# Performance work log

Measured on AMD Instinct MI355X. Metric: run time of the kernel, lower is better.

Reference implementation:

```python
import jax, jax.numpy as jnp
import numpy as np

B, N = 16, 131072
C_MID, C_OUT = 128, 16


def setup_inputs() -> dict:
    key = jax.random.key(0)
    k1, k2, k3, k4 = jax.random.split(key, 4)
    # points in roughly [-0.5, 0.5] so cube indexing covers the grids
    x = jax.random.uniform(k1, (B, N, 3), dtype=jnp.float32) - 0.5
    W1 = jax.random.normal(k2, (C_MID, 3), dtype=jnp.float32) * 0.1
    b1 = jnp.zeros((C_MID,), jnp.float32)
    W2 = jax.random.normal(k3, (C_OUT, C_MID), dtype=jnp.float32) * 0.1
    b2 = jnp.zeros((C_OUT,), jnp.float32)
    # fixed per-batch permutations (deterministic stand-in for torch.randperm)
    perm = jnp.stack([jax.random.permutation(jax.random.fold_in(k4, i), N)
                      for i in range(B)]).astype(jnp.int32)
    return {"x": x, "W1": W1, "b1": b1, "W2": W2, "b2": b2, "perm": perm}


def point_to_cell(pts, feat, W, H, D):
    # pts float [B,N,3] already clamped to [0, dim-1]; cast like torch LongTensor
    idx = pts.astype(jnp.int32)
    flat = (idx[..., 0] * H + idx[..., 1]) * D + idx[..., 2]  # [B,N]
    Bb, Nn, C = feat.shape

    def scatter_one(fi, fe):
        grid = jnp.zeros((W * H * D, C), feat.dtype)
        return grid.at[fi].set(fe)

    cell = jax.vmap(scatter_one)(flat, feat)           # [B, WHD, C]
    return cell.transpose(0, 2, 1).reshape(Bb, C, W, H, D)


def reference(x, W1, b1, W2, b2, perm):
    # PointNetfeatLocal: 1x1 Conv1d stack == per-point MLP 3 -> 128 -> 16
    h = jnp.maximum(jnp.einsum('bnc,hc->bnh', x, W1) + b1, 0.0)
    feat = jnp.einsum('bnh,oh->bno', h, W2) + b2       # [B,N,16]
    # shuffle_points_feat: per-batch permutation gather
    xs = jnp.take_along_axis(x, perm[..., None], axis=1)
    fs = jnp.take_along_axis(feat, perm[..., None], axis=1)
    # batch_grid_pooling32 / 64
    cube32 = jnp.clip(xs * 32.0 + 16.5, 0.0, 31.0)
    cube64 = jnp.clip(xs * 64.0 + 32.5, 0.0, 63.0)
    feat_cell32 = point_to_cell(cube32, fs, 32, 32, 32)  # [B,16,32,32,32]
    feat_cell64 = point_to_cell(cube64, fs, 64, 64, 64)  # [B,16,64,64,64]
    return feat_cell32, feat_cell64
```

## Files before the change

### kernel.cpp

```cpp
#include <hip/hip_runtime.h>

namespace {
constexpr int kB = 16;
constexpr int kN = 131072;
constexpr int kNLog = 17;
constexpr int kCMid = 128;
constexpr int kCOut = 16;
constexpr int kCells32Log = 15;
constexpr int kCells64Log = 18;
constexpr int kCells32 = 1 << kCells32Log;
constexpr int kCells64 = 1 << kCells64Log;
constexpr long kOut32Elems = (long)kB * kCOut * kCells32;
constexpr int kChunks32 = 16;
constexpr int kSlabs64 = 16;
constexpr int kSlabCells = kCells64 / kSlabs64;
}

typedef __bf16 bf16x8 __attribute__((ext_vector_type(8)));
typedef float f32x4 __attribute__((ext_vector_type(4)));

__device__ inline unsigned int packbf2(float lo, float hi) {
    unsigned int a = __float_as_uint(lo);
    unsigned int b = __float_as_uint(hi);
    a = (a + 0x7FFFu + ((a >> 16) & 1u)) >> 16;
    b = (b + 0x7FFFu + ((b >> 16) & 1u)) & 0xFFFF0000u;
    return b | a;
}
__device__ inline float bf_lo(unsigned int p) { return __uint_as_float(p << 16); }
__device__ inline float bf_hi(unsigned int p) { return __uint_as_float(p & 0xFFFF0000u); }

__device__ inline uint4 pack8(const float* h) {
    uint4 r;
    r.x = packbf2(h[0], h[1]); r.y = packbf2(h[2], h[3]);
    r.z = packbf2(h[4], h[5]); r.w = packbf2(h[6], h[7]);
    return r;
}

__global__ __launch_bounds__(256) void k_pack(
    const float* __restrict__ W1, const float* __restrict__ b1,
    const float* __restrict__ W2,
    float* __restrict__ W1p, uint4* __restrict__ w2h, uint4* __restrict__ w2l)
{
    const int t = threadIdx.x;
    for (int k = t; k < kCMid; k += 256) {
        W1p[k * 4 + 0] = W1[k * 3 + 0];
        W1p[k * 4 + 1] = W1[k * 3 + 1];
        W1p[k * 4 + 2] = W1[k * 3 + 2];
        W1p[k * 4 + 3] = b1[k];
    }
    {
        const int kw = t >> 6;
        const int lane = t & 63;
        const int ch = lane & 15;
        const int grp = lane >> 4;
        float v[8], lo[8];
        #pragma unroll
        for (int e = 0; e < 8; ++e)
            v[e] = W2[ch * kCMid + kw * 32 + grp * 8 + e];
        const uint4 hh = pack8(v);
        lo[0] = v[0] - bf_lo(hh.x); lo[1] = v[1] - bf_hi(hh.x);
        lo[2] = v[2] - bf_lo(hh.y); lo[3] = v[3] - bf_hi(hh.y);
        lo[4] = v[4] - bf_lo(hh.z); lo[5] = v[5] - bf_hi(hh.z);
        lo[6] = v[6] - bf_lo(hh.w); lo[7] = v[7] - bf_hi(hh.w);
        w2h[t] = hh;
        w2l[t] = pack8(lo);
    }
}

__global__ __launch_bounds__(256) void k_prec(
    const float* __restrict__ x,
    const int* __restrict__ perm,
    unsigned long long* __restrict__ prec)
{
    const long gid = (long)blockIdx.x * 256 + threadIdx.x;
    const long bbase = gid & ~(long)(kN - 1);
    const int i = (int)(gid & (kN - 1));
    const int j = perm[gid];

    const float* xp = x + (bbase + j) * 3;
    const float v0 = xp[0], v1 = xp[1], v2 = xp[2];

    const int ix32 = (int)fminf(fmaxf(__fadd_rn(__fmul_rn(v0, 32.0f), 16.5f), 0.0f), 31.0f);
    const int iy32 = (int)fminf(fmaxf(__fadd_rn(__fmul_rn(v1, 32.0f), 16.5f), 0.0f), 31.0f);
    const int iz32 = (int)fminf(fmaxf(__fadd_rn(__fmul_rn(v2, 32.0f), 16.5f), 0.0f), 31.0f);
    const int ix64 = (int)fminf(fmaxf(__fadd_rn(__fmul_rn(v0, 64.0f), 32.5f), 0.0f), 63.0f);
    const int iy64 = (int)fminf(fmaxf(__fadd_rn(__fmul_rn(v1, 64.0f), 32.5f), 0.0f), 63.0f);
    const int iz64 = (int)fminf(fmaxf(__fadd_rn(__fmul_rn(v2, 64.0f), 32.5f), 0.0f), 63.0f);

    const unsigned long long cell32 = (unsigned long long)((ix32 * 32 + iy32) * 32 + iz32);
    const unsigned long long cell64 = (unsigned long long)((ix64 * 64 + iy64) * 64 + iz64);
    prec[bbase + j] = (cell64 << 33) | (cell32 << 18) | (unsigned long long)(i + 1);
}

__global__ __launch_bounds__(256, 4) void k_mlp(
    const float* __restrict__ x,
    const float* __restrict__ W1p,
    const uint4* __restrict__ w2h, const uint4* __restrict__ w2l,
    const float* __restrict__ b2,
    uint2* __restrict__ feat)
{
    const int tid = threadIdx.x;
    const int lane = tid & 63;
    const int grp = lane >> 4;
    const int pt16 = lane & 15;
    const long base = (((long)blockIdx.x << 2) + (tid >> 6)) << 6;

    float xv[4][3];
    #pragma unroll
    for (int t = 0; t < 4; ++t) {
        const float* xp = x + (base + t * 16 + pt16) * 3;
        xv[t][0] = xp[0]; xv[t][1] = xp[1]; xv[t][2] = xp[2];
    }

    f32x4 acc[4];
    #pragma unroll
    for (int t = 0; t < 4; ++t) acc[t] = (f32x4){0.f, 0.f, 0.f, 0.f};

    const float4* __restrict__ w1v = (const float4*)W1p;

    #pragma unroll
    for (int kw = 0; kw < 4; ++kw) {
        const bf16x8 ah = __builtin_bit_cast(bf16x8, w2h[(kw << 6) + lane]);
        const bf16x8 al = __builtin_bit_cast(bf16x8, w2l[(kw << 6) + lane]);
        float4 w1r[8];
        #pragma unroll
        for (int e = 0; e < 8; ++e)
            w1r[e] = w1v[(kw << 5) + (grp << 3) + e];

        #pragma unroll
        for (int t = 0; t < 4; ++t) {
            float h[8], lo[8];
            #pragma unroll
            for (int e = 0; e < 8; ++e)
                h[e] = fmaxf(fmaf(w1r[e].x, xv[t][0],
                              fmaf(w1r[e].y, xv[t][1],
                               fmaf(w1r[e].z, xv[t][2], w1r[e].w))), 0.0f);
            const uint4 bh = pack8(h);
            lo[0] = h[0] - bf_lo(bh.x); lo[1] = h[1] - bf_hi(bh.x);
            lo[2] = h[2] - bf_lo(bh.y); lo[3] = h[3] - bf_hi(bh.y);
            lo[4] = h[4] - bf_lo(bh.z); lo[5] = h[5] - bf_hi(bh.z);
            lo[6] = h[6] - bf_lo(bh.w); lo[7] = h[7] - bf_hi(bh.w);
            const uint4 bl4 = pack8(lo);
            const bf16x8 bhv = __builtin_bit_cast(bf16x8, bh);
            const bf16x8 blv = __builtin_bit_cast(bf16x8, bl4);
            acc[t] = __builtin_amdgcn_mfma_f32_16x16x32_bf16(ah, bhv, acc[t], 0, 0, 0);
            acc[t] = __builtin_amdgcn_mfma_f32_16x16x32_bf16(ah, blv, acc[t], 0, 0, 0);
            acc[t] = __builtin_amdgcn_mfma_f32_16x16x32_bf16(al, bhv, acc[t], 0, 0, 0);
        }
    }

    const float4 bias = ((const float4*)b2)[grp];
    #pragma unroll
    for (int t = 0; t < 4; ++t) {
        const float c0 = acc[t][0] + bias.x;
        const float c1 = acc[t][1] + bias.y;
        const float c2 = acc[t][2] + bias.z;
        const float c3 = acc[t][3] + bias.w;
        uint2 o;
        o.x = packbf2(c0, c1);
        o.y = packbf2(c2, c3);
        feat[((base + t * 16 + pt16) << 2) + grp] = o;
    }
}

__global__ __launch_bounds__(1024) void k_win32(
    const unsigned long long* __restrict__ prec,
    unsigned int* __restrict__ partial32)
{
    __shared__ unsigned int lwin[kCells32];
    const int b = blockIdx.x >> 4;
    const int c = blockIdx.x & (kChunks32 - 1);
    const int t = threadIdx.x;

    #pragma unroll
    for (int r = 0; r < kCells32 / 1024; ++r) lwin[r * 1024 + t] = 0u;
    __syncthreads();

    const long base = ((long)b << kNLog) + (long)c * (kN / kChunks32);
    #pragma unroll
    for (int r = 0; r < (kN / kChunks32) / 1024; ++r) {
        const unsigned long long w = prec[base + r * 1024 + t];
        atomicMax(&lwin[(int)((w >> 18) & 0x7FFFull)], (unsigned int)(w & 0x3FFFFull));
    }
    __syncthreads();

    unsigned int* dst = partial32 + ((long)blockIdx.x << kCells32Log);
    #pragma unroll
    for (int r = 0; r < kCells32 / 1024; ++r) dst[r * 1024 + t] = lwin[r * 1024 + t];
}

__global__ __launch_bounds__(1024) void k_win64(
    const unsigned long long* __restrict__ prec,
    unsigned long long* __restrict__ win64)
{
    __shared__ unsigned long long lwin[kSlabCells];
    const int b = blockIdx.x >> 4;
    const int s = blockIdx.x & (kSlabs64 - 1);
    const int t = threadIdx.x;

    #pragma unroll
    for (int r = 0; r < kSlabCells / 1024; ++r) lwin[r * 1024 + t] = 0ull;
    __syncthreads();

    const long base = (long)b << kNLog;
    for (int r = 0; r < kN / 1024; ++r) {
        const int j = r * 1024 + t;
        const unsigned long long w = prec[base + j];
        const int cell = (int)(w >> 33);
        if ((cell >> 14) == s)
            atomicMax(&lwin[cell & (kSlabCells - 1)],
                      ((w & 0x3FFFFull) << 32) | (unsigned long long)(unsigned int)j);
    }
    __syncthreads();

    unsigned long long* dst = win64 + ((long)b << kCells64Log) + ((long)s << 14);
    #pragma unroll
    for (int r = 0; r < kSlabCells / 1024; ++r) dst[r * 1024 + t] = lwin[r * 1024 + t];
}

__global__ __launch_bounds__(256) void k_gather32(
    const unsigned int* __restrict__ partial32,
    const int* __restrict__ perm,
    const uint4* __restrict__ feat,
    float* __restrict__ out)
{
    const long gid = (long)blockIdx.x * 256 + threadIdx.x;
    const int b = (int)(gid >> kCells32Log);
    const int cell = (int)(gid & (kCells32 - 1));

    unsigned int w = 0u;
    #pragma unroll
    for (int c = 0; c < kChunks32; ++c)
        w = max(w, partial32[(((long)(b * kChunks32 + c)) << kCells32Log) + cell]);

    float v[kCOut];
    #pragma unroll
    for (int c = 0; c < kCOut; ++c) v[c] = 0.0f;

    if (w != 0u) {
        const int i = (int)(w - 1u);
        const int j = perm[((long)b << kNLog) + i];
        const long pidx = ((long)b << kNLog) + j;
        const uint4 f0 = feat[pidx * 2 + 0];
        const uint4 f1 = feat[pidx * 2 + 1];
        v[0]  = bf_lo(f0.x); v[1]  = bf_hi(f0.x);
        v[2]  = bf_lo(f0.y); v[3]  = bf_hi(f0.y);
        v[4]  = bf_lo(f0.z); v[5]  = bf_hi(f0.z);
        v[6]  = bf_lo(f0.w); v[7]  = bf_hi(f0.w);
        v[8]  = bf_lo(f1.x); v[9]  = bf_hi(f1.x);
        v[10] = bf_lo(f1.y); v[11] = bf_hi(f1.y);
        v[12] = bf_lo(f1.z); v[13] = bf_hi(f1.z);
        v[14] = bf_lo(f1.w); v[15] = bf_hi(f1.w);
    }

    float* op = out + (((long)b * kCOut) << kCells32Log) + cell;
    #pragma unroll
    for (int c = 0; c < kCOut; ++c) op[(long)c << kCells32Log] = v[c];
}

__global__ __launch_bounds__(256) void k_gather64(
    const unsigned long long* __restrict__ win,
    const uint4* __restrict__ feat,
    float* __restrict__ out)
{
    const long gid = (long)blockIdx.x * 256 + threadIdx.x;
    const int b = (int)(gid >> kCells64Log);
    const int cell = (int)(gid & (kCells64 - 1));
    const unsigned long long w = win[gid];

    float v[kCOut];
    #pragma unroll
    for (int c = 0; c < kCOut; ++c) v[c] = 0.0f;

    if (w != 0ull) {
        const int j = (int)(w & 0xFFFFFFFFull);
        const long pidx = ((long)b << kNLog) + j;
        const uint4 f0 = feat[pidx * 2 + 0];
        const uint4 f1 = feat[pidx * 2 + 1];
        v[0]  = bf_lo(f0.x); v[1]  = bf_hi(f0.x);
        v[2]  = bf_lo(f0.y); v[3]  = bf_hi(f0.y);
        v[4]  = bf_lo(f0.z); v[5]  = bf_hi(f0.z);
        v[6]  = bf_lo(f0.w); v[7]  = bf_hi(f0.w);
        v[8]  = bf_lo(f1.x); v[9]  = bf_hi(f1.x);
        v[10] = bf_lo(f1.y); v[11] = bf_hi(f1.y);
        v[12] = bf_lo(f1.z); v[13] = bf_hi(f1.z);
        v[14] = bf_lo(f1.w); v[15] = bf_hi(f1.w);
    }

    float* op = out + (((long)b * kCOut) << kCells64Log) + cell;
    #pragma unroll
    for (int c = 0; c < kCOut; ++c) op[(long)c << kCells64Log] = v[c];
}

extern "C" void kernel_launch(void* const* d_in, const int* in_sizes, int n_in,
                              void* d_out, int out_size, void* d_ws, size_t ws_size,
                              hipStream_t stream)
{
    const float* x  = (const float*)d_in[0];
    const float* W1 = (const float*)d_in[1];
    const float* b1 = (const float*)d_in[2];
    const float* W2 = (const float*)d_in[3];
    const float* b2 = (const float*)d_in[4];
    const int* perm = (const int*)d_in[5];

    float* out32 = (float*)d_out;
    float* out64 = out32 + kOut32Elems;

    float* W1p = (float*)d_ws;
    uint4* w2h = (uint4*)((char*)d_ws + 2048);
    uint4* w2l = w2h + 256;
    unsigned long long* prec = (unsigned long long*)((char*)d_ws + 16384);
    unsigned int* partial32 = (unsigned int*)(prec + (size_t)kB * kN);
    unsigned long long* win64 =
        (unsigned long long*)(partial32 + (size_t)kB * kChunks32 * kCells32);
    uint4* feat = (uint4*)(win64 + (size_t)kB * kCells64);

    const int nPtsBlocks = (int)(((long)kB * kN) / 256);
    const int n32Blocks  = (int)(((long)kB * kCells32) / 256);
    const int n64Blocks  = (int)(((long)kB * kCells64) / 256);
    dim3 blk(256);

    k_pack<<<1, 256, 0, stream>>>(W1, b1, W2, W1p, w2h, w2l);
    k_prec<<<nPtsBlocks, blk, 0, stream>>>(x, perm, prec);
    k_mlp<<<nPtsBlocks, blk, 0, stream>>>(x, W1p, w2h, w2l, b2, (uint2*)feat);

    k_win32<<<kB * kChunks32, 1024, 0, stream>>>(prec, partial32);
    k_win64<<<kB * kSlabs64, 1024, 0, stream>>>(prec, win64);

    k_gather32<<<n32Blocks, blk, 0, stream>>>(partial32, perm, feat, out32);
    k_gather64<<<n64Blocks, blk, 0, stream>>>(win64, feat, out64);
}
```

Measured before the change: 299.0 us.

## Replace packed 64-bit point records with inverse permutation and 32-bit cell keys

Result: slower. 316.3 us (+5.8%).

```diff
diff --git a/kernel.cpp b/kernel.cpp
--- a/kernel.cpp
+++ b/kernel.cpp
@@ -12,7 +12,7 @@
 constexpr int kCells64 = 1 << kCells64Log;
 constexpr long kOut32Elems = (long)kB * kCOut * kCells32;
 constexpr int kChunks32 = 16;
-constexpr int kSlabs64 = 16;
+constexpr int kSlabs64 = 8;
 constexpr int kSlabCells = kCells64 / kSlabs64;
 }
 
@@ -67,29 +67,25 @@
     }
 }
 
-__global__ __launch_bounds__(256) void k_prec(
+__global__ __launch_bounds__(256) void k_prep(
     const float* __restrict__ x,
     const int* __restrict__ perm,
-    unsigned long long* __restrict__ prec)
+    int* __restrict__ inv,
+    unsigned int* __restrict__ cell64)
 {
     const long gid = (long)blockIdx.x * 256 + threadIdx.x;
     const long bbase = gid & ~(long)(kN - 1);
     const int i = (int)(gid & (kN - 1));
     const int j = perm[gid];
-
-    const float* xp = x + (bbase + j) * 3;
-    const float v0 = xp[0], v1 = xp[1], v2 = xp[2];
-
-    const int ix32 = (int)fminf(fmaxf(__fadd_rn(__fmul_rn(v0, 32.0f), 16.5f), 0.0f), 31.0f);
-    const int iy32 = (int)fminf(fmaxf(__fadd_rn(__fmul_rn(v1, 32.0f), 16.5f), 0.0f), 31.0f);
-    const int iz32 = (int)fminf(fmaxf(__fadd_rn(__fmul_rn(v2, 32.0f), 16.5f), 0.0f), 31.0f);
+    inv[bbase + j] = i;
+
+    const float v0 = x[gid * 3 + 0];
+    const float v1 = x[gid * 3 + 1];
+    const float v2 = x[gid * 3 + 2];
     const int ix64 = (int)fminf(fmaxf(__fadd_rn(__fmul_rn(v0, 64.0f), 32.5f), 0.0f), 63.0f);
     const int iy64 = (int)fminf(fmaxf(__fadd_rn(__fmul_rn(v1, 64.0f), 32.5f), 0.0f), 63.0f);
     const int iz64 = (int)fminf(fmaxf(__fadd_rn(__fmul_rn(v2, 64.0f), 32.5f), 0.0f), 63.0f);
-
-    const unsigned long long cell32 = (unsigned long long)((ix32 * 32 + iy32) * 32 + iz32);
-    const unsigned long long cell64 = (unsigned long long)((ix64 * 64 + iy64) * 64 + iz64);
-    prec[bbase + j] = (cell64 << 33) | (cell32 << 18) | (unsigned long long)(i + 1);
+    cell64[gid] = (unsigned int)((ix64 * 64 + iy64) * 64 + iz64);
 }
 
 __global__ __launch_bounds__(256, 4) void k_mlp(
@@ -164,7 +160,8 @@
 }
 
 __global__ __launch_bounds__(1024) void k_win32(
-    const unsigned long long* __restrict__ prec,
+    const float* __restrict__ x,
+    const int* __restrict__ inv,
     unsigned int* __restrict__ partial32)
 {
     __shared__ unsigned int lwin[kCells32];
@@ -179,8 +176,15 @@
     const long base = ((long)b << kNLog) + (long)c * (kN / kChunks32);
     #pragma unroll
     for (int r = 0; r < (kN / kChunks32) / 1024; ++r) {
-        const unsigned long long w = prec[base + r * 1024 + t];
-        atomicMax(&lwin[(int)((w >> 18) & 0x7FFFull)], (unsigned int)(w & 0x3FFFFull));
+        const long j = base + r * 1024 + t;
+        const float v0 = x[j * 3 + 0];
+        const float v1 = x[j * 3 + 1];
+        const float v2 = x[j * 3 + 2];
+        const int ix = (int)fminf(fmaxf(__fadd_rn(__fmul_rn(v0, 32.0f), 16.5f), 0.0f), 31.0f);
+        const int iy = (int)fminf(fmaxf(__fadd_rn(__fmul_rn(v1, 32.0f), 16.5f), 0.0f), 31.0f);
+        const int iz = (int)fminf(fmaxf(__fadd_rn(__fmul_rn(v2, 32.0f), 16.5f), 0.0f), 31.0f);
+        const unsigned int pri = (unsigned int)(inv[j] + 1);
+        atomicMax(&lwin[(ix * 32 + iy) * 32 + iz], pri);
     }
     __syncthreads();
 
@@ -190,30 +194,30 @@
 }
 
 __global__ __launch_bounds__(1024) void k_win64(
-    const unsigned long long* __restrict__ prec,
-    unsigned long long* __restrict__ win64)
-{
-    __shared__ unsigned long long lwin[kSlabCells];
-    const int b = blockIdx.x >> 4;
+    const unsigned int* __restrict__ cell64,
+    const int* __restrict__ inv,
+    unsigned int* __restrict__ win64p)
+{
+    __shared__ unsigned int lwin[kSlabCells];
+    const int b = blockIdx.x >> 3;
     const int s = blockIdx.x & (kSlabs64 - 1);
     const int t = threadIdx.x;
 
     #pragma unroll
-    for (int r = 0; r < kSlabCells / 1024; ++r) lwin[r * 1024 + t] = 0ull;
+    for (int r = 0; r < kSlabCells / 1024; ++r) lwin[r * 1024 + t] = 0u;
     __syncthreads();
 
     const long base = (long)b << kNLog;
     for (int r = 0; r < kN / 1024; ++r) {
-        const int j = r * 1024 + t;
-        const unsigned long long w = prec[base + j];
-        const int cell = (int)(w >> 33);
-        if ((cell >> 14) == s)
-            atomicMax(&lwin[cell & (kSlabCells - 1)],
-                      ((w & 0x3FFFFull) << 32) | (unsigned long long)(unsigned int)j);
+        const long j = base + r * 1024 + t;
+        const unsigned int cell = cell64[j];
+        const unsigned int pri = (unsigned int)(inv[j] + 1);
+        if ((int)(cell >> 15) == s)
+            atomicMax(&lwin[cell & (kSlabCells - 1)], pri);
     }
     __syncthreads();
 
-    unsigned long long* dst = win64 + ((long)b << kCells64Log) + ((long)s << 14);
+    unsigned int* dst = win64p + ((long)b << kCells64Log) + ((long)s << 15);
     #pragma unroll
     for (int r = 0; r < kSlabCells / 1024; ++r) dst[r * 1024 + t] = lwin[r * 1024 + t];
 }
@@ -259,21 +263,23 @@
 }
 
 __global__ __launch_bounds__(256) void k_gather64(
-    const unsigned long long* __restrict__ win,
+    const unsigned int* __restrict__ win,
+    const int* __restrict__ perm,
     const uint4* __restrict__ feat,
     float* __restrict__ out)
 {
     const long gid = (long)blockIdx.x * 256 + threadIdx.x;
     const int b = (int)(gid >> kCells64Log);
     const int cell = (int)(gid & (kCells64 - 1));
-    const unsigned long long w = win[gid];
+    const unsigned int w = win[gid];
 
     float v[kCOut];
     #pragma unroll
     for (int c = 0; c < kCOut; ++c) v[c] = 0.0f;
 
-    if (w != 0ull) {
-        const int j = (int)(w & 0xFFFFFFFFull);
+    if (w != 0u) {
+        const int i = (int)(w - 1u);
+        const int j = perm[((long)b << kNLog) + i];
         const long pidx = ((long)b << kNLog) + j;
         const uint4 f0 = feat[pidx * 2 + 0];
         const uint4 f1 = feat[pidx * 2 + 1];
@@ -309,11 +315,11 @@
     float* W1p = (float*)d_ws;
     uint4* w2h = (uint4*)((char*)d_ws + 2048);
     uint4* w2l = w2h + 256;
-    unsigned long long* prec = (unsigned long long*)((char*)d_ws + 16384);
-    unsigned int* partial32 = (unsigned int*)(prec + (size_t)kB * kN);
-    unsigned long long* win64 =
-        (unsigned long long*)(partial32 + (size_t)kB * kChunks32 * kCells32);
-    uint4* feat = (uint4*)(win64 + (size_t)kB * kCells64);
+    int* inv = (int*)((char*)d_ws + 16384);
+    unsigned int* cell64 = (unsigned int*)(inv + (size_t)kB * kN);
+    unsigned int* partial32 = cell64 + (size_t)kB * kN;
+    unsigned int* win64p = partial32 + (size_t)kB * kChunks32 * kCells32;
+    uint4* feat = (uint4*)(win64p + (size_t)kB * kCells64);
 
     const int nPtsBlocks = (int)(((long)kB * kN) / 256);
     const int n32Blocks  = (int)(((long)kB * kCells32) / 256);
@@ -321,12 +327,12 @@
     dim3 blk(256);
 
     k_pack<<<1, 256, 0, stream>>>(W1, b1, W2, W1p, w2h, w2l);
-    k_prec<<<nPtsBlocks, blk, 0, stream>>>(x, perm, prec);
+    k_prep<<<nPtsBlocks, blk, 0, stream>>>(x, perm, inv, cell64);
     k_mlp<<<nPtsBlocks, blk, 0, stream>>>(x, W1p, w2h, w2l, b2, (uint2*)feat);
 
-    k_win32<<<kB * kChunks32, 1024, 0, stream>>>(prec, partial32);
-    k_win64<<<kB * kSlabs64, 1024, 0, stream>>>(prec, win64);
+    k_win32<<<kB * kChunks32, 1024, 0, stream>>>(x, inv, partial32);
+    k_win64<<<kB * kSlabs64, 1024, 0, stream>>>(cell64, inv, win64p);
 
     k_gather32<<<n32Blocks, blk, 0, stream>>>(partial32, perm, feat, out32);
-    k_gather64<<<n64Blocks, blk, 0, stream>>>(win64, feat, out64);
-}
+    k_gather64<<<n64Blocks, blk, 0, stream>>>(win64p, perm, feat, out64);
+}
```
